# Optimization experiments

Measured on AMD Instinct MI355X. Metric: run time of the kernel, lower is better.

## Reference

```python
import jax, jax.numpy as jnp
import numpy as np

WS = 7       # window_size
SHIFT = 3    # shift_size
NH = 4       # num_heads


def _layernorm(x, g, b, eps=1e-5):
    m = jnp.mean(x, axis=-1, keepdims=True)
    v = jnp.mean((x - m) ** 2, axis=-1, keepdims=True)
    return (x - m) * jax.lax.rsqrt(v + eps) * g + b


def _mha(x, wq, bq, wk, bk, wv, bv, wo, bo):
    # x: [n, s, c]; weights stored as [in, out]
    n, s, c = x.shape
    dk = c // NH
    q = (x @ wq + bq).reshape(n, s, NH, dk).transpose(0, 2, 1, 3)
    k = (x @ wk + bk).reshape(n, s, NH, dk).transpose(0, 2, 1, 3)
    v = (x @ wv + bv).reshape(n, s, NH, dk).transpose(0, 2, 1, 3)
    scores = jnp.einsum('nhqd,nhkd->nhqk', q, k) / jnp.sqrt(jnp.float32(dk))
    attn = jax.nn.softmax(scores, axis=-1)  # dropout is identity in eval
    out = jnp.einsum('nhqk,nhkd->nhqd', attn, v)
    out = out.transpose(0, 2, 1, 3).reshape(n, s, c)
    return out @ wo + bo


def _window_partition(x):
    B, H, W, C = x.shape
    x = x.reshape(B, H // WS, WS, W // WS, WS, C)
    x = x.transpose(0, 1, 3, 2, 4, 5)
    return x.reshape(-1, WS * WS, C)


def _window_reverse(wins, H, W):
    C = wins.shape[-1]
    B = wins.shape[0] // ((H // WS) * (W // WS))
    x = wins.reshape(B, H // WS, W // WS, WS, WS, C)
    x = x.transpose(0, 1, 3, 2, 4, 5)
    return x.reshape(B, H, W, C)


def setup_inputs() -> dict:
    key = jax.random.key(0)
    ks = jax.random.split(key, 16)
    C = 128
    def w(k, shape):
        return jax.random.normal(k, shape, dtype=jnp.float32) * 0.02
    return {
        'x':  jax.random.normal(ks[0], (4, 56, 56, C), dtype=jnp.float32),
        'wq': w(ks[1], (C, C)), 'bq': jnp.zeros((C,), jnp.float32),
        'wk': w(ks[2], (C, C)), 'bk': jnp.zeros((C,), jnp.float32),
        'wv': w(ks[3], (C, C)), 'bv': jnp.zeros((C,), jnp.float32),
        'wo': w(ks[4], (C, C)), 'bo': jnp.zeros((C,), jnp.float32),
        'w1': w(ks[5], (C, 4 * C)), 'b1': jnp.zeros((4 * C,), jnp.float32),
        'w2': w(ks[6], (4 * C, C)), 'b2': jnp.zeros((C,), jnp.float32),
        'g1': jnp.ones((C,), jnp.float32), 'be1': jnp.zeros((C,), jnp.float32),
        'g2': jnp.ones((C,), jnp.float32), 'be2': jnp.zeros((C,), jnp.float32),
    }


def reference(x, wq, bq, wk, bk, wv, bv, wo, bo, w1, b1, w2, b2, g1, be1, g2, be2):
    B, H, W, C = x.shape
    # cyclic shift
    xs = jnp.roll(x, shift=(-SHIFT, -SHIFT), axis=(1, 2)) if SHIFT > 0 else x
    # windowed attention (note: original code replaces x, no residual here)
    wins = _window_partition(xs)                         # [B*nW, 49, C]
    attn_wins = _mha(wins, wq, bq, wk, bk, wv, bv, wo, bo)
    xs = _window_reverse(attn_wins, H, W)
    x = jnp.roll(xs, shift=(SHIFT, SHIFT), axis=(1, 2)) if SHIFT > 0 else xs
    # global attention residual branch (flatten H*W tokens)
    xf = x.reshape(B, H * W, C)
    xf = xf + _mha(_layernorm(xf, g1, be1), wq, bq, wk, bk, wv, bv, wo, bo)
    # MLP residual branch
    h = jax.nn.gelu(_layernorm(xf, g2, be2) @ w1 + b1, approximate=False)
    xf = xf + (h @ w2 + b2)
    return xf.reshape(B, H, W, C)
```

## Files before the change

kernel.cpp:

```cpp
#include <hip/hip_runtime.h>
#include <hip/hip_bf16.h>
#include <math.h>

#define NH 4
#define DK 32
#define CC 128
#define HW 56
#define SHIFT 3
#define NTOK 12544
#define S_GLB 3136
#define VTW_STRIDE 12608
#define SCALE_L2E 0.25503488f

typedef unsigned short u16;
typedef short bf16x8 __attribute__((ext_vector_type(8)));
typedef unsigned short u16x8 __attribute__((ext_vector_type(8)));
typedef float f32x4 __attribute__((ext_vector_type(4)));

static __device__ __forceinline__ u16 f2bf(float f) {
  unsigned int b = __builtin_bit_cast(unsigned int, f);
  return (u16)((b + 0x7FFFu + ((b >> 16) & 1u)) >> 16);
}
static __device__ __forceinline__ unsigned pk2bf(float a, float b) {
  unsigned r;
  asm("v_cvt_pk_bf16_f32 %0, %1, %2" : "=v"(r) : "v"(a), "v"(b));
  return r;
}
static __device__ __forceinline__ float fexp2(float x) {
  float r;
  asm("v_exp_f32 %0, %1" : "=v"(r) : "v"(x));
  return r;
}
static __device__ __forceinline__ void gload16(const void* g, void* l) {
  __builtin_amdgcn_global_load_lds(
      (const __attribute__((address_space(1))) unsigned int*)g,
      (__attribute__((address_space(3))) unsigned int*)l, 16, 0, 0);
}

__global__ __launch_bounds__(256) void prep_k(
    const float* __restrict__ w1, const float* __restrict__ w2,
    const float* __restrict__ wq, const float* __restrict__ wk,
    const float* __restrict__ wv, const float* __restrict__ wo,
    const float* __restrict__ x,
    u16* __restrict__ w1t, u16* __restrict__ w2t,
    u16* __restrict__ wqkvt, u16* __restrict__ wot, u16* __restrict__ xg) {
  if (blockIdx.x < 768) {
    const int idx = blockIdx.x * 256 + threadIdx.x;
    if (idx < 65536) {
      const int c = idx >> 7, r = idx & 127;
      w1t[idx] = f2bf(w1[r * 512 + c]);
    } else if (idx < 131072) {
      const int o = idx - 65536;
      const int c = o / 512, r = o - c * 512;
      w2t[o] = f2bf(w2[r * 128 + c]);
    } else {
      const int o = idx - 131072;
      const int which = o >> 14, oo = o & 16383;
      const int c = oo >> 7, r = oo & 127;
      const float* src = (which == 0) ? wq : (which == 1) ? wk : (which == 2) ? wv : wo;
      u16* dst = (which < 3) ? (wqkvt + which * 16384) : wot;
      dst[oo] = f2bf(src[r * 128 + c]);
    }
  } else {
    const int bid = blockIdx.x - 768;
    const int t = bid * 2 + (threadIdx.x >> 7);
    const int c = threadIdx.x & 127;
    const int win = t / 49, tok = t % 49;
    const int b = win >> 6, wrem = win & 63;
    const int wi = wrem >> 3, wj = wrem & 7;
    const int i = tok / 7, j = tok % 7;
    int hh = wi * 7 + i + SHIFT; if (hh >= HW) hh -= HW;
    int ww = wj * 7 + j + SHIFT; if (ww >= HW) ww -= HW;
    xg[(size_t)t * CC + c] = f2bf(x[((size_t)(b * HW + hh) * HW + ww) * CC + c]);
  }
}

template <int PATH>
__global__ __launch_bounds__(256) void qkv_gemm_k(
    const u16* __restrict__ xin, const u16* __restrict__ wqkvt,
    const float* __restrict__ bq, const float* __restrict__ bk,
    const float* __restrict__ bv,
    u16* __restrict__ qo, u16* __restrict__ ko, u16* __restrict__ vto) {
  __shared__ __align__(16) u16 xs[64][136];
  __shared__ __align__(16) u16 wt[64][136];
  const int tid = threadIdx.x;
  const int w = tid >> 6, lane = tid & 63;
  const int lo = lane & 15, hi = lane >> 4, hi4 = hi * 4;
  const int m0 = blockIdx.x * 64;
  const int widx = blockIdx.y >> 1;
  const int n0 = (blockIdx.y & 1) * 64;
  {
    const int r = tid >> 2, sg = tid & 3;
    const u16* sx = &xin[(size_t)(m0 + r) * CC + sg * 32];
    const u16* sw = &wqkvt[(size_t)widx * CC * CC + (size_t)(n0 + r) * CC + sg * 32];
#pragma unroll
    for (int j = 0; j < 4; ++j) {
      *reinterpret_cast<u16x8*>(&xs[r][sg * 32 + j * 8]) = *reinterpret_cast<const u16x8*>(&sx[j * 8]);
      *reinterpret_cast<u16x8*>(&wt[r][sg * 32 + j * 8]) = *reinterpret_cast<const u16x8*>(&sw[j * 8]);
    }
  }
  __syncthreads();
  if (widx < 2) {
    const float* bias = (widx == 0) ? bq : bk;
    u16* outp = (widx == 0) ? qo : ko;
    const float oscale = (widx == 0) ? SCALE_L2E : 1.0f;
    f32x4 acc[4];
#pragma unroll
    for (int st = 0; st < 4; ++st) {
      const float b_ = bias[n0 + st * 16 + lo];
      acc[st] = (f32x4){b_, b_, b_, b_};
    }
#pragma unroll
    for (int kk = 0; kk < 4; ++kk) {
      const bf16x8 af = *reinterpret_cast<const bf16x8*>(&xs[w * 16 + lo][kk * 32 + 8 * hi]);
#pragma unroll
      for (int st = 0; st < 4; ++st) {
        const bf16x8 bfr = *reinterpret_cast<const bf16x8*>(&wt[st * 16 + lo][kk * 32 + 8 * hi]);
        acc[st] = __builtin_amdgcn_mfma_f32_16x16x32_bf16(af, bfr, acc[st], 0, 0, 0);
      }
    }
#pragma unroll
    for (int r = 0; r < 4; ++r) {
      const int mm = m0 + w * 16 + hi4 + r;
      size_t rowbase, hstride;
      if (PATH == 0) {
        const int win = mm / 49, tok = mm - win * 49;
        rowbase = ((size_t)(win * 4) * 49 + tok) * DK;
        hstride = (size_t)49 * DK;
      } else {
        const int b = mm / S_GLB, s = mm - b * S_GLB;
        rowbase = ((size_t)(b * 4) * S_GLB + s) * DK;
        hstride = (size_t)S_GLB * DK;
      }
#pragma unroll
      for (int st = 0; st < 4; ++st) {
        const int c = n0 + st * 16 + lo, h = c >> 5, d = c & 31;
        outp[rowbase + (size_t)h * hstride + d] = f2bf(acc[st][r] * oscale);
      }
    }
  } else {
    f32x4 bias4;
#pragma unroll
    for (int r = 0; r < 4; ++r) bias4[r] = bv[n0 + w * 16 + hi4 + r];
    f32x4 acc[4];
#pragma unroll
    for (int st = 0; st < 4; ++st) acc[st] = bias4;
#pragma unroll
    for (int kk = 0; kk < 4; ++kk) {
      const bf16x8 af = *reinterpret_cast<const bf16x8*>(&wt[w * 16 + lo][kk * 32 + 8 * hi]);
#pragma unroll
      for (int st = 0; st < 4; ++st) {
        const bf16x8 bfr = *reinterpret_cast<const bf16x8*>(&xs[st * 16 + lo][kk * 32 + 8 * hi]);
        acc[st] = __builtin_amdgcn_mfma_f32_16x16x32_bf16(af, bfr, acc[st], 0, 0, 0);
      }
    }
#pragma unroll
    for (int st = 0; st < 4; ++st) {
      const int mm = m0 + st * 16 + lo;
#pragma unroll
      for (int r = 0; r < 4; ++r) {
        const int c = n0 + w * 16 + hi4 + r;
        if (PATH == 0) {
          vto[(size_t)c * VTW_STRIDE + mm] = f2bf(acc[st][r]);
        } else {
          const int b = mm / S_GLB, s = mm - b * S_GLB;
          vto[((size_t)b * CC + c) * S_GLB + s] = f2bf(acc[st][r]);
        }
      }
    }
  }
}

__global__ __launch_bounds__(256) void win_attn_k(
    const u16* __restrict__ qw, const u16* __restrict__ kw,
    const u16* __restrict__ vtw, u16* __restrict__ aow) {
  __shared__ __align__(16) u16 psh[4][16][72];
  const int tid = threadIdx.x;
  const int wvi = tid >> 6, lane = tid & 63;
  const int lo = lane & 15, hi = lane >> 4, hi4 = hi * 4;
  const int wh = blockIdx.x * 4 + wvi;
  const int win = wh >> 2, hd = wh & 3;
  const f32x4 zero4 = {0.f, 0.f, 0.f, 0.f};
  bf16x8 ones;
#pragma unroll
  for (int j = 0; j < 8; ++j) ones[j] = (short)0x3F80;

  bf16x8 kf[4], vf[2][2];
#pragma unroll
  for (int st = 0; st < 4; ++st)
    kf[st] = *reinterpret_cast<const bf16x8*>(&kw[((size_t)wh * 49 + st * 16 + lo) * DK + 8 * hi]);
#pragma unroll
  for (int dst = 0; dst < 2; ++dst)
#pragma unroll
    for (int kch = 0; kch < 2; ++kch)
      vf[dst][kch] = *reinterpret_cast<const bf16x8*>(
          &vtw[(size_t)(hd * DK + dst * 16 + lo) * VTW_STRIDE + win * 49 + kch * 32 + 8 * hi]);

#pragma unroll
  for (int g = 0; g < 4; ++g) {
    const bf16x8 qf = *reinterpret_cast<const bf16x8*>(
        &qw[((size_t)wh * 49 + g * 16 + lo) * DK + 8 * hi]);
    f32x4 s4[4];
#pragma unroll
    for (int st = 0; st < 4; ++st) {
      s4[st] = __builtin_amdgcn_mfma_f32_16x16x32_bf16(kf[st], qf, zero4, 0, 0, 0);
#pragma unroll
      for (int r = 0; r < 4; ++r)
        if (st * 16 + hi4 + r >= 49) s4[st][r] = -1e30f;
    }
#pragma unroll
    for (int st = 0; st < 4; ++st) {
      uint2 pk;
      pk.x = pk2bf(fexp2(s4[st][0]), fexp2(s4[st][1]));
      pk.y = pk2bf(fexp2(s4[st][2]), fexp2(s4[st][3]));
      *reinterpret_cast<uint2*>(&psh[wvi][lo][st * 16 + hi4]) = pk;
    }
    asm volatile("" ::: "memory");
    f32x4 acc0 = zero4, acc1 = zero4, lacc = zero4;
#pragma unroll
    for (int kch = 0; kch < 2; ++kch) {
      const bf16x8 pa = *reinterpret_cast<const bf16x8*>(&psh[wvi][lo][kch * 32 + 8 * hi]);
      acc0 = __builtin_amdgcn_mfma_f32_16x16x32_bf16(pa, vf[0][kch], acc0, 0, 0, 0);
      acc1 = __builtin_amdgcn_mfma_f32_16x16x32_bf16(pa, vf[1][kch], acc1, 0, 0, 0);
      lacc = __builtin_amdgcn_mfma_f32_16x16x32_bf16(pa, ones, lacc, 0, 0, 0);
    }
#pragma unroll
    for (int r = 0; r < 4; ++r) {
      const int qrow = g * 16 + hi4 + r;
      if (qrow < 49) {
        const float rl = 1.0f / lacc[r];
        const size_t tw = (size_t)win * 49 + qrow;
        aow[tw * CC + hd * DK + lo] = f2bf(acc0[r] * rl);
        aow[tw * CC + hd * DK + 16 + lo] = f2bf(acc1[r] * rl);
      }
    }
  }
}

__global__ __launch_bounds__(256) void glb_attn_k(
    const u16* __restrict__ qg, const u16* __restrict__ kg,
    const u16* __restrict__ vtg, float* __restrict__ po, float* __restrict__ pl) {
  __shared__ __align__(16) u16 ksh[2][64][32];
  __shared__ __align__(16) u16 vtsh[2][32][64];
  __shared__ __align__(16) u16 psh[4][16][64];
  const int tid = threadIdx.x;
  const int w = tid >> 6, lane = tid & 63;
  const int lo = lane & 15, hi = lane >> 4, hi4 = hi * 4;
  const int wg = blockIdx.x;
  const int sid = (wg & 7) * 196 + (wg >> 3);
  const int sp = sid / 784;
  const int rem = sid - sp * 784;
  const int bh = rem / 49;
  const int q0 = (rem - bh * 49) * 64;
  const int kt_beg = sp * 25;
  const int kt_end = sp ? 49 : 25;
  const f32x4 zero4 = {0.f, 0.f, 0.f, 0.f};
  bf16x8 ones;
#pragma unroll
  for (int j = 0; j < 8; ++j) ones[j] = (short)0x3F80;

  const bf16x8 qfrag = *reinterpret_cast<const bf16x8*>(
      &qg[((size_t)bh * S_GLB + q0 + w * 16 + lo) * DK + 8 * hi]);
  const u16* kg0 = kg + (size_t)bh * S_GLB * DK;
  const u16* vg0 = vtg + (size_t)bh * DK * S_GLB;

  const u16* ksrc = kg0 + (size_t)(w * 16 + (lane >> 2)) * DK + (lane & 3) * 8;
  const u16* vsrc = vg0 + (size_t)(w * 8 + (lane >> 3)) * S_GLB + ((lane & 7) ^ (lane >> 3)) * 8;
  u16* kdst0 = &ksh[0][w * 16][0]; u16* kdst1 = &ksh[1][w * 16][0];
  u16* vdst0 = &vtsh[0][w * 8][0]; u16* vdst1 = &vtsh[1][w * 8][0];

  f32x4 oacc0 = zero4, oacc1 = zero4, lacc = zero4;

  gload16(ksrc + (size_t)kt_beg * 64 * DK, kdst0);
  gload16(vsrc + (size_t)kt_beg * 64, vdst0);
  __syncthreads();

  char* const pbase = (char*)&psh[w][lo][0];
  char* const vbase0 = (char*)&vtsh[0][0][0];
  const unsigned swz = (unsigned)(lo & 7) << 4;

  for (int kt = kt_beg; kt < kt_end; ++kt) {
    const int cur = (kt - kt_beg) & 1;
    if (kt + 1 < kt_end) {
      gload16(ksrc + (size_t)(kt + 1) * 64 * DK, cur ? kdst0 : kdst1);
      gload16(vsrc + (size_t)(kt + 1) * 64, cur ? vdst0 : vdst1);
    }
    f32x4 s4[4];
#pragma unroll
    for (int st = 0; st < 4; ++st) {
      const bf16x8 kfrag = *reinterpret_cast<const bf16x8*>(&ksh[cur][st * 16 + lo][8 * hi]);
      s4[st] = __builtin_amdgcn_mfma_f32_16x16x32_bf16(kfrag, qfrag, zero4, 0, 0, 0);
    }
#pragma unroll
    for (int st = 0; st < 4; ++st) {
      uint2 pk;
      pk.x = pk2bf(fexp2(s4[st][0]), fexp2(s4[st][1]));
      pk.y = pk2bf(fexp2(s4[st][2]), fexp2(s4[st][3]));
      *reinterpret_cast<uint2*>(pbase + (((unsigned)(st * 32 + hi * 8)) ^ swz)) = pk;
    }
    asm volatile("" ::: "memory");
    char* const vrow0 = vbase0 + (size_t)cur * (32 * 64 * 2) + lo * 128;
#pragma unroll
    for (int kch = 0; kch < 2; ++kch) {
      const unsigned off = ((unsigned)(kch * 64 + hi * 16)) ^ swz;
      const bf16x8 pa = *reinterpret_cast<const bf16x8*>(pbase + off);
      const bf16x8 v0 = *reinterpret_cast<const bf16x8*>(vrow0 + off);
      const bf16x8 v1 = *reinterpret_cast<const bf16x8*>(vrow0 + 16 * 128 + off);
      oacc0 = __builtin_amdgcn_mfma_f32_16x16x32_bf16(pa, v0, oacc0, 0, 0, 0);
      oacc1 = __builtin_amdgcn_mfma_f32_16x16x32_bf16(pa, v1, oacc1, 0, 0, 0);
      lacc = __builtin_amdgcn_mfma_f32_16x16x32_bf16(pa, ones, lacc, 0, 0, 0);
    }
    __syncthreads();
  }

  const int b = bh >> 2, hd = bh & 3;
  float* pob = po + (size_t)sp * NTOK * CC;
#pragma unroll
  for (int r = 0; r < 4; ++r) {
    const size_t t = (size_t)b * S_GLB + q0 + w * 16 + hi4 + r;
    pob[t * CC + hd * DK + lo] = oacc0[r];
    pob[t * CC + hd * DK + 16 + lo] = oacc1[r];
    if (lo == 0)
      pl[((size_t)sp * 16 + bh) * S_GLB + q0 + w * 16 + hi4 + r] = lacc[r];
  }
}

template <int MODE>
__global__ __launch_bounds__(256) void proj_ln_k(
    const u16* __restrict__ ain, const float* __restrict__ po,
    const float* __restrict__ pl, const u16* __restrict__ wot,
    const float* __restrict__ bo, const float* __restrict__ resid,
    const float* __restrict__ lng, const float* __restrict__ lnb,
    float* __restrict__ xfo, u16* __restrict__ ybf) {
  __shared__ __align__(16) u16 xs[64][136];
  __shared__ __align__(16) u16 wt[128][136];
  const int tid = threadIdx.x;
  const int w = tid >> 6, lane = tid & 63;
  const int lo = lane & 15, hi = lane >> 4, hi4 = hi * 4;
  const int m0 = blockIdx.x * 64;
  {
    const int r = tid >> 2, sg = tid & 3;
    if (MODE == 0) {
      const u16* sx = &ain[(size_t)(m0 + r) * CC + sg * 32];
#pragma unroll
      for (int j = 0; j < 4; ++j)
        *reinterpret_cast<u16x8*>(&xs[r][sg * 32 + j * 8]) = *reinterpret_cast<const u16x8*>(&sx[j * 8]);
    } else {
      const int mm = m0 + r;
      const int b = mm / S_GLB, s_ = mm - b * S_GLB;
      const float l0 = pl[((size_t)(b * 4 + sg)) * S_GLB + s_];
      const float l1 = pl[((size_t)(16 + b * 4 + sg)) * S_GLB + s_];
      const float rl = 1.0f / (l0 + l1);
      const float* pa = &po[(size_t)mm * CC + sg * 32];
      const float* pb = pa + (size_t)NTOK * CC;
#pragma unroll
      for (int j = 0; j < 32; j += 4) {
        const float4 a4 = *reinterpret_cast<const float4*>(&pa[j]);
        const float4 b4 = *reinterpret_cast<const float4*>(&pb[j]);
        uint2 pk;
        pk.x = pk2bf((a4.x + b4.x) * rl, (a4.y + b4.y) * rl);
        pk.y = pk2bf((a4.z + b4.z) * rl, (a4.w + b4.w) * rl);
        *reinterpret_cast<uint2*>(&xs[r][sg * 32 + j]) = pk;
      }
    }
    const int r2 = tid >> 1, sg2 = tid & 1;
    const u16* sw = &wot[(size_t)r2 * CC + sg2 * 64];
#pragma unroll
    for (int j = 0; j < 8; ++j)
      *reinterpret_cast<u16x8*>(&wt[r2][sg2 * 64 + j * 8]) = *reinterpret_cast<const u16x8*>(&sw[j * 8]);
  }
  __syncthreads();
  f32x4 acc[8];
#pragma unroll
  for (int st = 0; st < 8; ++st) {
    const float b_ = bo[st * 16 + lo];
    acc[st] = (f32x4){b_, b_, b_, b_};
  }
#pragma unroll
  for (int kk = 0; kk < 4; ++kk) {
    const bf16x8 af = *reinterpret_cast<const bf16x8*>(&xs[w * 16 + lo][kk * 32 + 8 * hi]);
#pragma unroll
    for (int st = 0; st < 8; ++st) {
      const bf16x8 bfr = *reinterpret_cast<const bf16x8*>(&wt[st * 16 + lo][kk * 32 + 8 * hi]);
      acc[st] = __builtin_amdgcn_mfma_f32_16x16x32_bf16(af, bfr, acc[st], 0, 0, 0);
    }
  }
  float gv[8], bv2[8];
#pragma unroll
  for (int st = 0; st < 8; ++st) { gv[st] = lng[st * 16 + lo]; bv2[st] = lnb[st * 16 + lo]; }
#pragma unroll
  for (int r = 0; r < 4; ++r) {
    const int mm = m0 + w * 16 + hi4 + r;
    size_t trow;
    if (MODE == 0) {
      const int win = mm / 49, tok = mm - win * 49;
      const int b = win >> 6, wi = (win >> 3) & 7, wj = win & 7;
      const int ii = tok / 7, jj = tok - ii * 7;
      int hr = wi * 7 + ii + SHIFT; if (hr >= HW) hr -= HW;
      int wr = wj * 7 + jj + SHIFT; if (wr >= HW) wr -= HW;
      trow = (size_t)b * S_GLB + hr * HW + wr;
    } else {
      trow = (size_t)mm;
    }
    float v[8];
    float s = 0.f, sq = 0.f;
#pragma unroll
    for (int st = 0; st < 8; ++st) {
      float t_ = acc[st][r];
      if (MODE == 1) t_ += resid[trow * CC + st * 16 + lo];
      v[st] = t_;
      s += t_;
      sq += t_ * t_;
    }
    s += __shfl_xor(s, 1); s += __shfl_xor(s, 2); s += __shfl_xor(s, 4); s += __shfl_xor(s, 8);
    sq += __shfl_xor(sq, 1); sq += __shfl_xor(sq, 2); sq += __shfl_xor(sq, 4); sq += __shfl_xor(sq, 8);
    const float mu = s * 0.0078125f;
    const float rsig = rsqrtf(sq * 0.0078125f - mu * mu + 1e-5f);
#pragma unroll
    for (int st = 0; st < 8; ++st) {
      const size_t idx = trow * CC + st * 16 + lo;
      xfo[idx] = v[st];
      ybf[idx] = f2bf((v[st] - mu) * rsig * gv[st] + bv2[st]);
    }
  }
}

__global__ __launch_bounds__(256) void gemm1_k(
    const u16* __restrict__ ybf, const u16* __restrict__ w1t,
    const float* __restrict__ b1, u16* __restrict__ hb) {
  __shared__ __align__(16) u16 xs[64][136];
  __shared__ __align__(16) u16 wt[64][136];
  const int tid = threadIdx.x;
  const int w = tid >> 6, lane = tid & 63;
  const int lo = lane & 15, hi = lane >> 4;
  const int m0 = blockIdx.x * 64, n0 = blockIdx.y * 64;
  {
    const int r = tid >> 2, sg = tid & 3;
    const u16* src_x = &ybf[(size_t)(m0 + r) * CC + sg * 32];
    const u16* src_w = &w1t[(size_t)(n0 + r) * CC + sg * 32];
#pragma unroll
    for (int j = 0; j < 4; ++j) {
      *reinterpret_cast<u16x8*>(&xs[r][sg * 32 + j * 8]) = *reinterpret_cast<const u16x8*>(&src_x[j * 8]);
      *reinterpret_cast<u16x8*>(&wt[r][sg * 32 + j * 8]) = *reinterpret_cast<const u16x8*>(&src_w[j * 8]);
    }
  }
  __syncthreads();
  f32x4 acc[4];
#pragma unroll
  for (int st = 0; st < 4; ++st) {
    const float bv = b1[n0 + st * 16 + lo];
    acc[st] = (f32x4){bv, bv, bv, bv};
  }
#pragma unroll
  for (int kk = 0; kk < 4; ++kk) {
    const bf16x8 af = *reinterpret_cast<const bf16x8*>(&xs[w * 16 + lo][kk * 32 + 8 * hi]);
#pragma unroll
    for (int st = 0; st < 4; ++st) {
      const bf16x8 bfr = *reinterpret_cast<const bf16x8*>(&wt[st * 16 + lo][kk * 32 + 8 * hi]);
      acc[st] = __builtin_amdgcn_mfma_f32_16x16x32_bf16(af, bfr, acc[st], 0, 0, 0);
    }
  }
#pragma unroll
  for (int st = 0; st < 4; ++st) {
#pragma unroll
    for (int r = 0; r < 4; ++r) {
      const float val = acc[st][r];
      const float gel = 0.5f * val * (1.0f + erff(val * 0.70710678118f));
      hb[(size_t)(m0 + w * 16 + (hi << 2) + r) * 512 + n0 + st * 16 + lo] = f2bf(gel);
    }
  }
}

__global__ __launch_bounds__(256) void gemm2_k(
    const u16* __restrict__ hb, const u16* __restrict__ w2t,
    const float* __restrict__ b2, const float* __restrict__ xf,
    float* __restrict__ out) {
  __shared__ __align__(16) u16 xs[64][136];
  __shared__ __align__(16) u16 wt[64][136];
  const int tid = threadIdx.x;
  const int w = tid >> 6, lane = tid & 63;
  const int lo = lane & 15, hi = lane >> 4;
  const int m0 = blockIdx.x * 64, n0 = blockIdx.y * 64;
  f32x4 acc[4];
#pragma unroll
  for (int st = 0; st < 4; ++st) {
    const float bv = b2[n0 + st * 16 + lo];
    acc[st] = (f32x4){bv, bv, bv, bv};
  }
  for (int kc = 0; kc < 4; ++kc) {
    if (kc) __syncthreads();
    {
      const int r = tid >> 2, sg = tid & 3;
      const u16* src_x = &hb[(size_t)(m0 + r) * 512 + kc * 128 + sg * 32];
      const u16* src_w = &w2t[(size_t)(n0 + r) * 512 + kc * 128 + sg * 32];
#pragma unroll
      for (int j = 0; j < 4; ++j) {
        *reinterpret_cast<u16x8*>(&xs[r][sg * 32 + j * 8]) = *reinterpret_cast<const u16x8*>(&src_x[j * 8]);
        *reinterpret_cast<u16x8*>(&wt[r][sg * 32 + j * 8]) = *reinterpret_cast<const u16x8*>(&src_w[j * 8]);
      }
    }
    __syncthreads();
#pragma unroll
    for (int kk = 0; kk < 4; ++kk) {
      const bf16x8 af = *reinterpret_cast<const bf16x8*>(&xs[w * 16 + lo][kk * 32 + 8 * hi]);
#pragma unroll
      for (int st = 0; st < 4; ++st) {
        const bf16x8 bfr = *reinterpret_cast<const bf16x8*>(&wt[st * 16 + lo][kk * 32 + 8 * hi]);
        acc[st] = __builtin_amdgcn_mfma_f32_16x16x32_bf16(af, bfr, acc[st], 0, 0, 0);
      }
    }
  }
#pragma unroll
  for (int st = 0; st < 4; ++st) {
#pragma unroll
    for (int r = 0; r < 4; ++r) {
      const size_t idx = (size_t)(m0 + w * 16 + (hi << 2) + r) * CC + n0 + st * 16 + lo;
      out[idx] = xf[idx] + acc[st][r];
    }
  }
}

extern "C" void kernel_launch(void* const* d_in, const int* in_sizes, int n_in,
                              void* d_out, int out_size, void* d_ws, size_t ws_size,
                              hipStream_t stream) {
  (void)in_sizes; (void)n_in; (void)out_size; (void)ws_size;
  const float* x   = (const float*)d_in[0];
  const float* wq  = (const float*)d_in[1];
  const float* bq  = (const float*)d_in[2];
  const float* wk  = (const float*)d_in[3];
  const float* bk  = (const float*)d_in[4];
  const float* wv  = (const float*)d_in[5];
  const float* bv  = (const float*)d_in[6];
  const float* wo  = (const float*)d_in[7];
  const float* bo  = (const float*)d_in[8];
  const float* w1  = (const float*)d_in[9];
  const float* b1  = (const float*)d_in[10];
  const float* w2  = (const float*)d_in[11];
  const float* b2  = (const float*)d_in[12];
  const float* g1  = (const float*)d_in[13];
  const float* be1 = (const float*)d_in[14];
  const float* g2  = (const float*)d_in[15];
  const float* be2 = (const float*)d_in[16];
  float* out = (float*)d_out;

  char* p = (char*)d_ws;
  auto alloc = [&](size_t bytes) { char* r = p; p += (bytes + 255) & ~(size_t)255; return r; };
  float* xf  = (float*)alloc((size_t)NTOK * CC * 4);
  u16* xg    = (u16*)alloc((size_t)NTOK * CC * 2);
  u16* qw    = (u16*)alloc((size_t)NTOK * CC * 2 + 4096);
  u16* kw    = (u16*)alloc((size_t)NTOK * CC * 2 + 4096);
  u16* vtw   = (u16*)alloc((size_t)CC * VTW_STRIDE * 2);
  u16* aow   = (u16*)alloc((size_t)NTOK * CC * 2);
  u16* hb    = (u16*)alloc((size_t)NTOK * 512 * 2);
  float* po  = (float*)alloc((size_t)2 * NTOK * CC * 4);
  float* pl  = (float*)alloc((size_t)2 * 16 * S_GLB * 4);
  u16* wqkvt = (u16*)alloc(3 * 16384 * 2);
  u16* wot   = (u16*)alloc(16384 * 2);
  u16* w1t   = (u16*)alloc(65536 * 2);
  u16* w2t   = (u16*)alloc(65536 * 2);

  prep_k<<<768 + NTOK / 2, 256, 0, stream>>>(
      w1, w2, wq, wk, wv, wo, x, w1t, w2t, wqkvt, wot, xg);
  qkv_gemm_k<0><<<dim3(NTOK / 64, 6), 256, 0, stream>>>(xg, wqkvt, bq, bk, bv, qw, kw, vtw);
  win_attn_k<<<256, 256, 0, stream>>>(qw, kw, vtw, aow);
  proj_ln_k<0><<<NTOK / 64, 256, 0, stream>>>(
      aow, nullptr, nullptr, wot, bo, nullptr, g1, be1, xf, xg);
  qkv_gemm_k<1><<<dim3(NTOK / 64, 6), 256, 0, stream>>>(xg, wqkvt, bq, bk, bv, qw, kw, vtw);
  glb_attn_k<<<1568, 256, 0, stream>>>(qw, kw, vtw, po, pl);
  proj_ln_k<1><<<NTOK / 64, 256, 0, stream>>>(
      nullptr, po, pl, wot, bo, xf, g2, be2, xf, xg);
  gemm1_k<<<dim3(NTOK / 64, 8), 256, 0, stream>>>(xg, w1t, b1, hb);
  gemm2_k<<<dim3(NTOK / 64, 2), 256, 0, stream>>>(hb, w2t, b2, xf, out);
}
```

Before: 112.9 us.

## Halve global-attention block to two waves each handling 32 query rows

The global attention kernel now launches 128 threads per block instead of 256. Each wave processes two 16-row query tiles and reuses the same K fragments and V tiles from shared memory for both, so there are fewer LDS reads of K/V per unit of work. Each thread now issues two K and two V global loads per tile to keep the 64-key tile loading intact. This costs more registers per wave (double accumulators and score arrays) and gives fewer waves per block to hide memory latency.

```diff
diff --git a/kernel.cpp b/kernel.cpp
--- a/kernel.cpp
+++ b/kernel.cpp
@@ -237,12 +237,12 @@
   }
 }
 
-__global__ __launch_bounds__(256) void glb_attn_k(
+__global__ __launch_bounds__(128) void glb_attn_k(
     const u16* __restrict__ qg, const u16* __restrict__ kg,
     const u16* __restrict__ vtg, float* __restrict__ po, float* __restrict__ pl) {
   __shared__ __align__(16) u16 ksh[2][64][32];
   __shared__ __align__(16) u16 vtsh[2][32][64];
-  __shared__ __align__(16) u16 psh[4][16][64];
+  __shared__ __align__(16) u16 psh[2][2][16][64];
   const int tid = threadIdx.x;
   const int w = tid >> 6, lane = tid & 63;
   const int lo = lane & 15, hi = lane >> 4, hi4 = hi * 4;
@@ -259,56 +259,80 @@
 #pragma unroll
   for (int j = 0; j < 8; ++j) ones[j] = (short)0x3F80;
 
-  const bf16x8 qfrag = *reinterpret_cast<const bf16x8*>(
-      &qg[((size_t)bh * S_GLB + q0 + w * 16 + lo) * DK + 8 * hi]);
+  const bf16x8 qf0 = *reinterpret_cast<const bf16x8*>(
+      &qg[((size_t)bh * S_GLB + q0 + w * 32 + lo) * DK + 8 * hi]);
+  const bf16x8 qf1 = *reinterpret_cast<const bf16x8*>(
+      &qg[((size_t)bh * S_GLB + q0 + w * 32 + 16 + lo) * DK + 8 * hi]);
   const u16* kg0 = kg + (size_t)bh * S_GLB * DK;
   const u16* vg0 = vtg + (size_t)bh * DK * S_GLB;
 
-  const u16* ksrc = kg0 + (size_t)(w * 16 + (lane >> 2)) * DK + (lane & 3) * 8;
-  const u16* vsrc = vg0 + (size_t)(w * 8 + (lane >> 3)) * S_GLB + ((lane & 7) ^ (lane >> 3)) * 8;
-  u16* kdst0 = &ksh[0][w * 16][0]; u16* kdst1 = &ksh[1][w * 16][0];
-  u16* vdst0 = &vtsh[0][w * 8][0]; u16* vdst1 = &vtsh[1][w * 8][0];
-
-  f32x4 oacc0 = zero4, oacc1 = zero4, lacc = zero4;
-
-  gload16(ksrc + (size_t)kt_beg * 64 * DK, kdst0);
-  gload16(vsrc + (size_t)kt_beg * 64, vdst0);
+  const u16* ksrc = kg0 + (size_t)(w * 32 + (lane >> 2)) * DK + (lane & 3) * 8;
+  const u16* vsrc = vg0 + (size_t)(w * 16 + (lane >> 3)) * S_GLB + ((lane & 7) ^ (lane >> 3)) * 8;
+  u16* const kdst[2] = {&ksh[0][w * 32][0], &ksh[1][w * 32][0]};
+  u16* const vdst[2] = {&vtsh[0][w * 16][0], &vtsh[1][w * 16][0]};
+
+  f32x4 oacc00 = zero4, oacc01 = zero4, lacc0 = zero4;
+  f32x4 oacc10 = zero4, oacc11 = zero4, lacc1 = zero4;
+
+  {
+    const size_t ko = (size_t)kt_beg * 64 * DK, vo = (size_t)kt_beg * 64;
+    gload16(ksrc + ko, kdst[0]);
+    gload16(ksrc + ko + 16 * DK, kdst[0] + 16 * 32);
+    gload16(vsrc + vo, vdst[0]);
+    gload16(vsrc + vo + 8 * S_GLB, vdst[0] + 8 * 64);
+  }
   __syncthreads();
 
-  char* const pbase = (char*)&psh[w][lo][0];
+  char* const pbase0 = (char*)&psh[w][0][lo][0];
+  char* const pbase1 = (char*)&psh[w][1][lo][0];
   char* const vbase0 = (char*)&vtsh[0][0][0];
   const unsigned swz = (unsigned)(lo & 7) << 4;
 
   for (int kt = kt_beg; kt < kt_end; ++kt) {
     const int cur = (kt - kt_beg) & 1;
     if (kt + 1 < kt_end) {
-      gload16(ksrc + (size_t)(kt + 1) * 64 * DK, cur ? kdst0 : kdst1);
-      gload16(vsrc + (size_t)(kt + 1) * 64, cur ? vdst0 : vdst1);
-    }
-    f32x4 s4[4];
+      const size_t ko = (size_t)(kt + 1) * 64 * DK, vo = (size_t)(kt + 1) * 64;
+      gload16(ksrc + ko, kdst[cur ^ 1]);
+      gload16(ksrc + ko + 16 * DK, kdst[cur ^ 1] + 16 * 32);
+      gload16(vsrc + vo, vdst[cur ^ 1]);
+      gload16(vsrc + vo + 8 * S_GLB, vdst[cur ^ 1] + 8 * 64);
+    }
+    bf16x8 kf[4];
+#pragma unroll
+    for (int st = 0; st < 4; ++st)
+      kf[st] = *reinterpret_cast<const bf16x8*>(&ksh[cur][st * 16 + lo][8 * hi]);
+    f32x4 s40[4], s41[4];
 #pragma unroll
     for (int st = 0; st < 4; ++st) {
-      const bf16x8 kfrag = *reinterpret_cast<const bf16x8*>(&ksh[cur][st * 16 + lo][8 * hi]);
-      s4[st] = __builtin_amdgcn_mfma_f32_16x16x32_bf16(kfrag, qfrag, zero4, 0, 0, 0);
+      s40[st] = __builtin_amdgcn_mfma_f32_16x16x32_bf16(kf[st], qf0, zero4, 0, 0, 0);
+      s41[st] = __builtin_amdgcn_mfma_f32_16x16x32_bf16(kf[st], qf1, zero4, 0, 0, 0);
     }
 #pragma unroll
     for (int st = 0; st < 4; ++st) {
-      uint2 pk;
-      pk.x = pk2bf(fexp2(s4[st][0]), fexp2(s4[st][1]));
-      pk.y = pk2bf(fexp2(s4[st][2]), fexp2(s4[st][3]));
-      *reinterpret_cast<uint2*>(pbase + (((unsigned)(st * 32 + hi * 8)) ^ swz)) = pk;
+      uint2 pk0, pk1;
+      pk0.x = pk2bf(fexp2(s40[st][0]), fexp2(s40[st][1]));
+      pk0.y = pk2bf(fexp2(s40[st][2]), fexp2(s40[st][3]));
+      pk1.x = pk2bf(fexp2(s41[st][0]), fexp2(s41[st][1]));
+      pk1.y = pk2bf(fexp2(s41[st][2]), fexp2(s41[st][3]));
+      const unsigned off = ((unsigned)(st * 32 + hi * 8)) ^ swz;
+      *reinterpret_cast<uint2*>(pbase0 + off) = pk0;
+      *reinterpret_cast<uint2*>(pbase1 + off) = pk1;
     }
     asm volatile("" ::: "memory");
     char* const vrow0 = vbase0 + (size_t)cur * (32 * 64 * 2) + lo * 128;
 #pragma unroll
     for (int kch = 0; kch < 2; ++kch) {
       const unsigned off = ((unsigned)(kch * 64 + hi * 16)) ^ swz;
-      const bf16x8 pa = *reinterpret_cast<const bf16x8*>(pbase + off);
       const bf16x8 v0 = *reinterpret_cast<const bf16x8*>(vrow0 + off);
       const bf16x8 v1 = *reinterpret_cast<const bf16x8*>(vrow0 + 16 * 128 + off);
-      oacc0 = __builtin_amdgcn_mfma_f32_16x16x32_bf16(pa, v0, oacc0, 0, 0, 0);
-      oacc1 = __builtin_amdgcn_mfma_f32_16x16x32_bf16(pa, v1, oacc1, 0, 0, 0);
-      lacc = __builtin_amdgcn_mfma_f32_16x16x32_bf16(pa, ones, lacc, 0, 0, 0);
+      const bf16x8 pa0 = *reinterpret_cast<const bf16x8*>(pbase0 + off);
+      const bf16x8 pa1 = *reinterpret_cast<const bf16x8*>(pbase1 + off);
+      oacc00 = __builtin_amdgcn_mfma_f32_16x16x32_bf16(pa0, v0, oacc00, 0, 0, 0);
+      oacc01 = __builtin_amdgcn_mfma_f32_16x16x32_bf16(pa0, v1, oacc01, 0, 0, 0);
+      lacc0 = __builtin_amdgcn_mfma_f32_16x16x32_bf16(pa0, ones, lacc0, 0, 0, 0);
+      oacc10 = __builtin_amdgcn_mfma_f32_16x16x32_bf16(pa1, v0, oacc10, 0, 0, 0);
+      oacc11 = __builtin_amdgcn_mfma_f32_16x16x32_bf16(pa1, v1, oacc11, 0, 0, 0);
+      lacc1 = __builtin_amdgcn_mfma_f32_16x16x32_bf16(pa1, ones, lacc1, 0, 0, 0);
     }
     __syncthreads();
   }
@@ -317,11 +341,16 @@
   float* pob = po + (size_t)sp * NTOK * CC;
 #pragma unroll
   for (int r = 0; r < 4; ++r) {
-    const size_t t = (size_t)b * S_GLB + q0 + w * 16 + hi4 + r;
-    pob[t * CC + hd * DK + lo] = oacc0[r];
-    pob[t * CC + hd * DK + 16 + lo] = oacc1[r];
-    if (lo == 0)
-      pl[((size_t)sp * 16 + bh) * S_GLB + q0 + w * 16 + hi4 + r] = lacc[r];
+    const size_t t0 = (size_t)b * S_GLB + q0 + w * 32 + hi4 + r;
+    pob[t0 * CC + hd * DK + lo] = oacc00[r];
+    pob[t0 * CC + hd * DK + 16 + lo] = oacc01[r];
+    const size_t t1 = t0 + 16;
+    pob[t1 * CC + hd * DK + lo] = oacc10[r];
+    pob[t1 * CC + hd * DK + 16 + lo] = oacc11[r];
+    if (lo == 0) {
+      pl[((size_t)sp * 16 + bh) * S_GLB + q0 + w * 32 + hi4 + r] = lacc0[r];
+      pl[((size_t)sp * 16 + bh) * S_GLB + q0 + w * 32 + 16 + hi4 + r] = lacc1[r];
+    }
   }
 }
 
@@ -566,7 +595,7 @@
   proj_ln_k<0><<<NTOK / 64, 256, 0, stream>>>(
       aow, nullptr, nullptr, wot, bo, nullptr, g1, be1, xf, xg);
   qkv_gemm_k<1><<<dim3(NTOK / 64, 6), 256, 0, stream>>>(xg, wqkvt, bq, bk, bv, qw, kw, vtw);
-  glb_attn_k<<<1568, 256, 0, stream>>>(qw, kw, vtw, po, pl);
+  glb_attn_k<<<1568, 128, 0, stream>>>(qw, kw, vtw, po, pl);
   proj_ln_k<1><<<NTOK / 64, 256, 0, stream>>>(
       nullptr, po, pl, wot, bo, xf, g2, be2, xf, xg);
   gemm1_k<<<dim3(NTOK / 64, 8), 256, 0, stream>>>(xg, w1t, b1, hb);
```

After: 119.7 us. +6.1%, slower.
